# Kernel tuning notes

Measured on AMD Instinct MI355X. Metric: run time of the kernel, lower is better.

## Reference

```python
import jax, jax.numpy as jnp
import numpy as np

D_MODEL = 512
NHEAD = 8
HEAD_DIM = D_MODEL // NHEAD
D_FF = 2048
EPS = 1e-5


def _linear_params(key, d_in, d_out):
    kw, kb = jax.random.split(key)
    bound = 1.0 / np.sqrt(d_in)
    W = jax.random.uniform(kw, (d_out, d_in), jnp.float32, -bound, bound)
    b = jax.random.uniform(kb, (d_out,), jnp.float32, -bound, bound)
    return W, b


def setup_inputs() -> dict:
    key = jax.random.key(0)
    ks = jax.random.split(key, 8)
    src = jax.random.normal(ks[0], (4, 2048, D_MODEL), jnp.float32)
    Wq, bq = _linear_params(ks[1], D_MODEL, D_MODEL)
    Wk, bk = _linear_params(ks[2], D_MODEL, D_MODEL)
    Wv, bv = _linear_params(ks[3], D_MODEL, D_MODEL)
    Wo, bo = _linear_params(ks[4], D_MODEL, D_MODEL)
    W1, b1 = _linear_params(ks[5], D_MODEL, D_FF)
    W2, b2 = _linear_params(ks[6], D_FF, D_MODEL)
    g1 = jnp.ones((D_MODEL,), jnp.float32)
    be1 = jnp.zeros((D_MODEL,), jnp.float32)
    g2 = jnp.ones((D_MODEL,), jnp.float32)
    be2 = jnp.zeros((D_MODEL,), jnp.float32)
    return dict(src=src, Wq=Wq, bq=bq, Wk=Wk, bk=bk, Wv=Wv, bv=bv,
                Wo=Wo, bo=bo, W1=W1, b1=b1, W2=W2, b2=b2,
                g1=g1, be1=be1, g2=g2, be2=be2)


def _layer_norm(x, g, b):
    mu = jnp.mean(x, axis=-1, keepdims=True)
    var = jnp.mean(jnp.square(x - mu), axis=-1, keepdims=True)
    return (x - mu) / jnp.sqrt(var + EPS) * g + b


def reference(src, Wq, bq, Wk, bk, Wv, bv, Wo, bo, W1, b1, W2, b2, g1, be1, g2, be2):
    B, T, D = src.shape
    scale = np.sqrt(HEAD_DIM).astype(np.float32)
    # Projections (torch Linear: x @ W.T + b)
    Q = (src @ Wq.T + bq).reshape(B, T, NHEAD, HEAD_DIM).transpose(0, 2, 1, 3)
    K = (src @ Wk.T + bk).reshape(B, T, NHEAD, HEAD_DIM).transpose(0, 2, 1, 3)
    V = (src @ Wv.T + bv).reshape(B, T, NHEAD, HEAD_DIM).transpose(0, 2, 1, 3)
    # Explicit QK^T -> softmax -> V (no mask, dropout=0)
    scores = jnp.einsum('bhqd,bhkd->bhqk', Q, K) / scale  # (B,H,T,T)
    attn = jax.nn.softmax(scores, axis=-1)
    ctx = jnp.einsum('bhqk,bhkd->bhqd', attn, V)
    ctx = ctx.transpose(0, 2, 1, 3).reshape(B, T, D)
    attn_out = ctx @ Wo.T + bo
    # Add & Norm 1
    x = _layer_norm(src + attn_out, g1, be1)
    # FFN: Linear -> GELU -> Linear
    h = jax.nn.gelu(x @ W1.T + b1, approximate=False)
    ffn_out = h @ W2.T + b2
    # Add & Norm 2
    return _layer_norm(x + ffn_out, g2, be2)
```

## Files before the change

kernel.cpp:

```cpp
#include <hip/hip_runtime.h>
#include <hip/hip_bf16.h>
#include <math.h>

typedef __bf16 bf16_t;
typedef __bf16 bf16x8 __attribute__((ext_vector_type(8)));
typedef __bf16 bf16x2 __attribute__((ext_vector_type(2)));
typedef float  f32x4  __attribute__((ext_vector_type(4)));

#define D_MODEL 512
#define NHEAD   8
#define HD      64
#define D_FF    2048
#define TOKENS  8192
#define SEQ     2048
#define BATCH   4

__device__ __forceinline__ void gload16(const bf16_t* g, bf16_t* l)
{
    __builtin_amdgcn_global_load_lds(
        (const __attribute__((address_space(1))) void*)g,
        (__attribute__((address_space(3))) void*)l,
        16, 0, 0);
}

__device__ __forceinline__ void cvt4(const float* s, bf16_t* d)
{
    float4 v = *(const float4*)s;
    alignas(8) bf16_t t[4] = {(bf16_t)v.x, (bf16_t)v.y, (bf16_t)v.z, (bf16_t)v.w};
    *(uint2*)d = *(const uint2*)t;
}

__global__ void cvt_weights(const float* __restrict__ Wq, const float* __restrict__ Wk,
                            const float* __restrict__ Wv, const float* __restrict__ Wo,
                            const float* __restrict__ W1, const float* __restrict__ W2,
                            const float* __restrict__ bq, const float* __restrict__ bk,
                            const float* __restrict__ bv,
                            bf16_t* __restrict__ Wqkvb, bf16_t* __restrict__ Wob,
                            bf16_t* __restrict__ W1b, bf16_t* __restrict__ W2b,
                            float* __restrict__ bqkv, float* __restrict__ zbias)
{
    int i = blockIdx.x * 256 + threadIdx.x;
    if (i < 65536)        cvt4(Wq + (size_t)i * 4,            Wqkvb + (size_t)i * 4);
    else if (i < 131072)  cvt4(Wk + (size_t)(i - 65536) * 4,  Wqkvb + (size_t)i * 4);
    else if (i < 196608)  cvt4(Wv + (size_t)(i - 131072) * 4, Wqkvb + (size_t)i * 4);
    else if (i < 262144)  cvt4(Wo + (size_t)(i - 196608) * 4, Wob + (size_t)(i - 196608) * 4);
    else if (i < 524288)  cvt4(W1 + (size_t)(i - 262144) * 4, W1b + (size_t)(i - 262144) * 4);
    else if (i < 786432)  cvt4(W2 + (size_t)(i - 524288) * 4, W2b + (size_t)(i - 524288) * 4);
    else if (i < 786816) {
        int j = i - 786432;
        const float* s = (j < 128) ? bq + j * 4 : (j < 256) ? bk + (j - 128) * 4
                                                            : bv + (j - 256) * 4;
        *(float4*)(bqkv + (j & 127) * 4 + (j >> 7) * 512) = *(const float4*)s;
    } else if (i < 786944) {
        int j = i - 786816;
        *(float4*)(zbias + j * 4) = make_float4(0.f, 0.f, 0.f, 0.f);
    }
}

template <int BM, int EPI, bool AF32, bool SPLIT2>
__global__ __launch_bounds__(256)
void gemm_bt(const void* __restrict__ Ain, const bf16_t* __restrict__ B,
             const float* __restrict__ bias, const float* __restrict__ biasz,
             void* __restrict__ Cout, int M, int N, int K)
{
    constexpr int MI = BM / 32;
    __shared__ bf16_t sA[BM][32];
    __shared__ bf16_t sB[128][32];
    bf16_t* sAf = &sA[0][0];
    bf16_t* sBf = &sB[0][0];

    const int tid  = threadIdx.x;
    const int wave = tid >> 6;
    const int lane = tid & 63;
    const int g    = lane >> 4;
    const int c16  = lane & 15;
    const int wm   = (wave >> 1) * (BM / 2);
    const int wn   = (wave & 1) * 64;
    const int m0   = blockIdx.y * BM;
    const int n0   = blockIdx.x * 128;

    const int zz    = SPLIT2 ? blockIdx.z : 0;
    const int Keff  = SPLIT2 ? (K >> 1) : K;
    const int kbase = zz * Keff;
    const float* bptr = (SPLIT2 && zz) ? biasz : bias;

    const f32x4 fz = {0.f, 0.f, 0.f, 0.f};
    f32x4 acc[MI][4];
#pragma unroll
    for (int i = 0; i < MI; i++)
#pragma unroll
        for (int j = 0; j < 4; j++) acc[i][j] = fz;

    const int srow = tid >> 2;
    const int scol = (tid & 3) * 8;
    const bf16_t* pa  = AF32 ? nullptr : (const bf16_t*)Ain + (size_t)(m0 + srow) * K + kbase + scol;
    const float*  paf = AF32 ? (const float*)Ain + (size_t)(m0 + srow) * K + kbase + scol : nullptr;
    const bf16_t* pb  = B + (size_t)(n0 + srow) * K + kbase + scol;

    for (int k0 = 0; k0 < Keff; k0 += 32) {
        float4 ua[BM / 64][2];
        if (AF32) {
#pragma unroll
            for (int i = 0; i < BM / 64; i++) {
                ua[i][0] = *(const float4*)(paf + (size_t)i * 64 * K + k0);
                ua[i][1] = *(const float4*)(paf + (size_t)i * 64 * K + k0 + 4);
            }
        }
        __syncthreads();
        if (AF32) {
#pragma unroll
            for (int i = 0; i < BM / 64; i++) {
                alignas(16) bf16_t t[8];
#pragma unroll
                for (int j = 0; j < 4; j++) {
                    t[j]     = (bf16_t)((const float*)&ua[i][0])[j];
                    t[j + 4] = (bf16_t)((const float*)&ua[i][1])[j];
                }
                *(int4*)(sAf + i * 2048 + tid * 8) = *(const int4*)t;
            }
        } else {
#pragma unroll
            for (int i = 0; i < BM / 64; i++)
                gload16(pa + (size_t)i * 64 * K + k0, sAf + i * 2048 + tid * 8);
        }
#pragma unroll
        for (int i = 0; i < 2; i++)
            gload16(pb + (size_t)i * 64 * K + k0, sBf + i * 2048 + tid * 8);
        __syncthreads();

        bf16x8 af[MI], bfr[4];
#pragma unroll
        for (int i = 0; i < MI; i++)
            af[i] = *(const bf16x8*)&sA[wm + i * 16 + c16][g * 8];
#pragma unroll
        for (int j = 0; j < 4; j++)
            bfr[j] = *(const bf16x8*)&sB[wn + j * 16 + c16][g * 8];
#pragma unroll
        for (int mi = 0; mi < MI; mi++)
#pragma unroll
            for (int ni = 0; ni < 4; ni++)
                acc[mi][ni] = __builtin_amdgcn_mfma_f32_16x16x32_bf16(
                    af[mi], bfr[ni], acc[mi][ni], 0, 0, 0);
    }

    float* outf = (float*)Cout + (size_t)zz * M * N;
#pragma unroll
    for (int mi = 0; mi < MI; mi++) {
#pragma unroll
        for (int ni = 0; ni < 4; ni++) {
            const int col = n0 + wn + ni * 16 + c16;
            const float bv = bptr[col];
#pragma unroll
            for (int r = 0; r < 4; r++) {
                const int row = m0 + wm + mi * 16 + g * 4 + r;
                float v = acc[mi][ni][r] + bv;
                if (EPI == 1) v = 0.5f * v * (1.f + erff(v * 0.70710678118654752f));
                if (EPI == 2)
                    outf[(size_t)row * N + col] = v;
                else
                    ((bf16_t*)Cout)[(size_t)row * N + col] = (bf16_t)v;
            }
        }
    }
}

__global__ __launch_bounds__(256)
void transpose_v(const bf16_t* __restrict__ qkv, bf16_t* __restrict__ vt)
{
    __shared__ bf16_t st[64][72];
    const int t0 = blockIdx.x * 64;
    const int bh = blockIdx.y;
    const int b = bh >> 3, h = bh & 7;
    const int tid = threadIdx.x;

    for (int c = tid; c < 512; c += 256) {
        int r = c >> 3, cj = (c & 7) * 8;
        const bf16_t* src = qkv + ((size_t)(b * SEQ + t0 + r)) * 1536 + 1024 + h * 64 + cj;
        *(int4*)&st[r][cj] = *(const int4*)src;
    }
    __syncthreads();
    for (int c = tid; c < 512; c += 256) {
        int d = c >> 3, pj = (c & 7) * 8;
        alignas(16) bf16_t tmp[8];
#pragma unroll
        for (int j = 0; j < 8; j++) {
            int p = pj + j;
            int t = (p & 32) + ((p & 1) << 4) + ((p & 31) >> 1);
            tmp[j] = st[t][d];
        }
        *(int4*)(vt + ((size_t)(bh * 64 + d)) * SEQ + t0 + pj) = *(const int4*)tmp;
    }
}

__global__ __launch_bounds__(256)
void flash_attn(const bf16_t* __restrict__ qkv, const bf16_t* __restrict__ vt,
                bf16_t* __restrict__ ctx)
{
    __shared__ bf16_t sK[2][64][64];
    __shared__ bf16_t sVt[2][64][64];
    __shared__ bf16_t sOnes[16][72];
    __shared__ bf16_t sP[128][72];

    const int bh = blockIdx.y;
    const int b = bh >> 3, h = bh & 7;
    const int q0 = blockIdx.x * 128;
    const int tid = threadIdx.x;
    const int wave = tid >> 6, lane = tid & 63;
    const int g = lane >> 4, c16 = lane & 15;

    for (int c = tid; c < 16 * 72; c += 256)
        sOnes[c / 72][c % 72] = (c / 72 == 0) ? (bf16_t)1.0f : (bf16_t)0.0f;

    const float qscale = 0.125f * 1.4426950408889634f;
    bf16x8 aq[2][2];
#pragma unroll
    for (int mf = 0; mf < 2; mf++)
#pragma unroll
        for (int ks = 0; ks < 2; ks++) {
            bf16x8 v = *(const bf16x8*)(qkv +
                ((size_t)(b * SEQ + q0 + wave * 32 + mf * 16 + c16)) * 1536 +
                h * 64 + ks * 32 + g * 8);
#pragma unroll
            for (int j = 0; j < 8; j++) v[j] = (bf16_t)((float)v[j] * qscale);
            aq[mf][ks] = v;
        }

    const f32x4 fz = {0.f, 0.f, 0.f, 0.f};
    f32x4 acc_o[2][5];
#pragma unroll
    for (int mf = 0; mf < 2; mf++)
#pragma unroll
        for (int nd = 0; nd < 5; nd++) acc_o[mf][nd] = fz;

    const int f0 = tid,        r0 = f0 >> 3, l0 = (f0 & 7) ^ (r0 & 7);
    const int f1 = tid + 256,  r1 = f1 >> 3, l1 = (f1 & 7) ^ (r1 & 7);
    const bf16_t* gK0 = qkv + ((size_t)(b * SEQ + r0)) * 1536 + 512 + h * 64 + l0 * 8;
    const bf16_t* gK1 = qkv + ((size_t)(b * SEQ + r1)) * 1536 + 512 + h * 64 + l1 * 8;
    const bf16_t* gV0 = vt + ((size_t)(bh * 64 + r0)) * SEQ + l0 * 8;
    const bf16_t* gV1 = vt + ((size_t)(bh * 64 + r1)) * SEQ + l1 * 8;
    bf16_t* lK = &sK[0][0][0];
    bf16_t* lV = &sVt[0][0][0];

    gload16(gK0, lK + f0 * 8);
    gload16(gK1, lK + f1 * 8);
    gload16(gV0, lV + f0 * 8);
    gload16(gV1, lV + f1 * 8);

    for (int it = 0; it < 32; ++it) {
        const int cur = it & 1;
        __syncthreads();
        if (it < 31) {
            const size_t kv = (size_t)(it + 1) * 64;
            const int bo = (cur ^ 1) * 4096;
            gload16(gK0 + kv * 1536, lK + bo + f0 * 8);
            gload16(gK1 + kv * 1536, lK + bo + f1 * 8);
            gload16(gV0 + kv,        lV + bo + f0 * 8);
            gload16(gV1 + kv,        lV + bo + f1 * 8);
        }

        f32x4 accs[2][4];
#pragma unroll
        for (int mf = 0; mf < 2; mf++)
#pragma unroll
            for (int n = 0; n < 4; n++) accs[mf][n] = fz;
#pragma unroll
        for (int ks = 0; ks < 2; ks++)
#pragma unroll
            for (int n = 0; n < 4; n++) {
                const int pc = ((ks * 4 + g) ^ (c16 & 7)) * 8;
                bf16x8 bk = *(const bf16x8*)&sK[cur][n * 16 + c16][pc];
                accs[0][n] = __builtin_amdgcn_mfma_f32_16x16x32_bf16(aq[0][ks], bk, accs[0][n], 0, 0, 0);
                accs[1][n] = __builtin_amdgcn_mfma_f32_16x16x32_bf16(aq[1][ks], bk, accs[1][n], 0, 0, 0);
            }

#pragma unroll
        for (int mf = 0; mf < 2; mf++)
#pragma unroll
            for (int r = 0; r < 4; r++) {
                const int prow = wave * 32 + mf * 16 + g * 4 + r;
#pragma unroll
                for (int ks = 0; ks < 2; ks++) {
                    bf16x2 pp;
                    pp[0] = (bf16_t)__builtin_amdgcn_exp2f(accs[mf][2 * ks][r]);
                    pp[1] = (bf16_t)__builtin_amdgcn_exp2f(accs[mf][2 * ks + 1][r]);
                    *(bf16x2*)&sP[prow][ks * 32 + 2 * c16] = pp;
                }
            }

#pragma unroll
        for (int ks = 0; ks < 2; ks++) {
            bf16x8 ap0 = *(const bf16x8*)&sP[wave * 32 + c16][ks * 32 + g * 8];
            bf16x8 ap1 = *(const bf16x8*)&sP[wave * 32 + 16 + c16][ks * 32 + g * 8];
#pragma unroll
            for (int nd = 0; nd < 5; nd++) {
                bf16x8 vb;
                if (nd < 4) {
                    const int pc = ((ks * 4 + g) ^ (c16 & 7)) * 8;
                    vb = *(const bf16x8*)&sVt[cur][nd * 16 + c16][pc];
                } else {
                    vb = *(const bf16x8*)&sOnes[c16][ks * 32 + g * 8];
                }
                acc_o[0][nd] = __builtin_amdgcn_mfma_f32_16x16x32_bf16(ap0, vb, acc_o[0][nd], 0, 0, 0);
                acc_o[1][nd] = __builtin_amdgcn_mfma_f32_16x16x32_bf16(ap1, vb, acc_o[1][nd], 0, 0, 0);
            }
        }
    }

#pragma unroll
    for (int mf = 0; mf < 2; mf++)
#pragma unroll
        for (int r = 0; r < 4; r++) {
            float lv  = __shfl(acc_o[mf][4][r], lane & 48, 64);
            float inv = 1.0f / lv;
            const size_t base =
                ((size_t)(b * SEQ + q0 + wave * 32 + mf * 16 + g * 4 + r)) * 512 + h * 64;
#pragma unroll
            for (int nd = 0; nd < 4; nd++)
                ctx[base + nd * 16 + c16] = (bf16_t)(acc_o[mf][nd][r] * inv);
        }
}

__global__ __launch_bounds__(256)
void add_ln3(const float* __restrict__ a, const float* __restrict__ b,
             const float* __restrict__ c,
             const float* __restrict__ gamma, const float* __restrict__ beta,
             float* __restrict__ outf, bf16_t* __restrict__ outb)
{
    const int row  = blockIdx.x * 4 + (threadIdx.x >> 6);
    const int lane = threadIdx.x & 63;
    const size_t base = (size_t)row * 512 + lane * 8;

    float v[8];
#pragma unroll
    for (int h = 0; h < 2; h++) {
        float4 av = *(const float4*)(a + base + h * 4);
        float4 bv = *(const float4*)(b + base + h * 4);
        float4 cv = *(const float4*)(c + base + h * 4);
        v[h * 4 + 0] = av.x + bv.x + cv.x;
        v[h * 4 + 1] = av.y + bv.y + cv.y;
        v[h * 4 + 2] = av.z + bv.z + cv.z;
        v[h * 4 + 3] = av.w + bv.w + cv.w;
    }

    float s = 0.f;
#pragma unroll
    for (int i = 0; i < 8; i++) s += v[i];
#pragma unroll
    for (int off = 32; off > 0; off >>= 1) s += __shfl_xor(s, off);
    const float mu = s * (1.f / 512.f);

    float q = 0.f;
#pragma unroll
    for (int i = 0; i < 8; i++) { float d = v[i] - mu; q += d * d; }
#pragma unroll
    for (int off = 32; off > 0; off >>= 1) q += __shfl_xor(q, off);
    const float rstd = rsqrtf(q * (1.f / 512.f) + 1e-5f);

    float4 g0 = *(const float4*)(gamma + lane * 8);
    float4 g1 = *(const float4*)(gamma + lane * 8 + 4);
    float4 e0 = *(const float4*)(beta + lane * 8);
    float4 e1 = *(const float4*)(beta + lane * 8 + 4);
    const float gg[8] = {g0.x, g0.y, g0.z, g0.w, g1.x, g1.y, g1.z, g1.w};
    const float ee[8] = {e0.x, e0.y, e0.z, e0.w, e1.x, e1.y, e1.z, e1.w};

    float o[8];
#pragma unroll
    for (int i = 0; i < 8; i++) o[i] = (v[i] - mu) * rstd * gg[i] + ee[i];

    *(float4*)(outf + base)     = make_float4(o[0], o[1], o[2], o[3]);
    *(float4*)(outf + base + 4) = make_float4(o[4], o[5], o[6], o[7]);
    if (outb) {
        alignas(16) bf16_t ob[8];
#pragma unroll
        for (int i = 0; i < 8; i++) ob[i] = (bf16_t)o[i];
        *(int4*)(outb + base) = *(const int4*)ob;
    }
}

extern "C" void kernel_launch(void* const* d_in, const int* in_sizes, int n_in,
                              void* d_out, int out_size, void* d_ws, size_t ws_size,
                              hipStream_t stream)
{
    const float* src = (const float*)d_in[0];
    const float* Wq  = (const float*)d_in[1];  const float* bq  = (const float*)d_in[2];
    const float* Wk  = (const float*)d_in[3];  const float* bk  = (const float*)d_in[4];
    const float* Wv  = (const float*)d_in[5];  const float* bv  = (const float*)d_in[6];
    const float* Wo  = (const float*)d_in[7];  const float* bo  = (const float*)d_in[8];
    const float* W1  = (const float*)d_in[9];  const float* b1  = (const float*)d_in[10];
    const float* W2  = (const float*)d_in[11]; const float* b2  = (const float*)d_in[12];
    const float* g1  = (const float*)d_in[13]; const float* be1 = (const float*)d_in[14];
    const float* g2  = (const float*)d_in[15]; const float* be2 = (const float*)d_in[16];
    float* out = (float*)d_out;

    char* ws = (char*)d_ws;
    size_t off = 0;
    auto alloc = [&](size_t bytes) -> void* {
        void* p = ws + off;
        off = (off + bytes + 255) & ~(size_t)255;
        return p;
    };

    bf16_t* Wqkvb = (bf16_t*)alloc((size_t)1536 * 512 * 2);
    bf16_t* Wob   = (bf16_t*)alloc((size_t)512 * 512 * 2);
    bf16_t* W1b   = (bf16_t*)alloc((size_t)2048 * 512 * 2);
    bf16_t* W2b   = (bf16_t*)alloc((size_t)512 * 2048 * 2);
    float*  bqkv  = (float*)alloc(1536 * 4);
    float*  zbias = (float*)alloc(512 * 4);
    bf16_t* QKV   = (bf16_t*)alloc((size_t)TOKENS * 1536 * 2);
    bf16_t* Vt    = (bf16_t*)alloc((size_t)32 * 64 * SEQ * 2);
    bf16_t* CTX   = (bf16_t*)alloc((size_t)TOKENS * 512 * 2);
    float*  ATTa  = (float*)alloc((size_t)TOKENS * 512 * 4);
    float*  ATTb  = (float*)alloc((size_t)TOKENS * 512 * 4);
    float*  X1    = (float*)alloc((size_t)TOKENS * 512 * 4);
    bf16_t* X1b   = (bf16_t*)alloc((size_t)TOKENS * 512 * 2);

    bf16_t* H    = QKV;
    float*  FFNa = ATTa;
    float*  FFNb = ATTb;

    cvt_weights<<<3074, 256, 0, stream>>>(Wq, Wk, Wv, Wo, W1, W2, bq, bk, bv,
                                          Wqkvb, Wob, W1b, W2b, bqkv, zbias);

    gemm_bt<128, 0, true, false><<<dim3(12, 64), 256, 0, stream>>>(
        src, Wqkvb, bqkv, zbias, QKV, TOKENS, 1536, 512);

    transpose_v<<<dim3(32, 32), 256, 0, stream>>>(QKV, Vt);
    flash_attn<<<dim3(16, 32), 256, 0, stream>>>(QKV, Vt, CTX);

    gemm_bt<64, 2, false, true><<<dim3(4, 128, 2), 256, 0, stream>>>(
        CTX, Wob, bo, zbias, ATTa, TOKENS, 512, 512);

    add_ln3<<<2048, 256, 0, stream>>>(src, ATTa, ATTb, g1, be1, X1, X1b);

    gemm_bt<128, 1, false, false><<<dim3(16, 64), 256, 0, stream>>>(
        X1b, W1b, b1, zbias, H, TOKENS, 2048, 512);

    gemm_bt<64, 2, false, true><<<dim3(4, 128, 2), 256, 0, stream>>>(
        H, W2b, b2, zbias, FFNa, TOKENS, 512, 2048);

    add_ln3<<<2048, 256, 0, stream>>>(X1, FFNa, FFNb, g2, be2, out, nullptr);
}
```

Measured before the change: 309.2 us.

## Double-buffer GEMM LDS tiles and pre-convert src to bf16 in conversion kernel

The GEMM kernel gets a two-stage LDS ping-pong buffer. Async global-to-LDS loads for the next K tile are issued before the MFMA work on the current tile, and there is one barrier per iteration instead of two. To keep every GEMM on this path, src is now converted to bf16 inside the weight-conversion kernel, which removes the fp32 A-operand variant. This costs twice the LDS per block and an extra bf16 copy of src written and read through global memory. The code relies on the compiler inserting the needed vmcnt waits before the barrier for global_load_lds, which is a correctness risk.

Measured after the change: 296.5 us. -4.1%, faster.

```diff
diff --git a/kernel.cpp b/kernel.cpp
--- a/kernel.cpp
+++ b/kernel.cpp
@@ -30,16 +30,20 @@
     *(uint2*)d = *(const uint2*)t;
 }
 
-__global__ void cvt_weights(const float* __restrict__ Wq, const float* __restrict__ Wk,
+__global__ void cvt_weights(const float* __restrict__ src,
+                            const float* __restrict__ Wq, const float* __restrict__ Wk,
                             const float* __restrict__ Wv, const float* __restrict__ Wo,
                             const float* __restrict__ W1, const float* __restrict__ W2,
                             const float* __restrict__ bq, const float* __restrict__ bk,
                             const float* __restrict__ bv,
+                            bf16_t* __restrict__ Xb,
                             bf16_t* __restrict__ Wqkvb, bf16_t* __restrict__ Wob,
                             bf16_t* __restrict__ W1b, bf16_t* __restrict__ W2b,
                             float* __restrict__ bqkv, float* __restrict__ zbias)
 {
     int i = blockIdx.x * 256 + threadIdx.x;
+    if (i < 1048576) { cvt4(src + (size_t)i * 4, Xb + (size_t)i * 4); return; }
+    i -= 1048576;
     if (i < 65536)        cvt4(Wq + (size_t)i * 4,            Wqkvb + (size_t)i * 4);
     else if (i < 131072)  cvt4(Wk + (size_t)(i - 65536) * 4,  Wqkvb + (size_t)i * 4);
     else if (i < 196608)  cvt4(Wv + (size_t)(i - 131072) * 4, Wqkvb + (size_t)i * 4);
@@ -57,17 +61,17 @@
     }
 }
 
-template <int BM, int EPI, bool AF32, bool SPLIT2>
+template <int BM, int EPI, bool SPLIT2>
 __global__ __launch_bounds__(256)
-void gemm_bt(const void* __restrict__ Ain, const bf16_t* __restrict__ B,
+void gemm_bt(const bf16_t* __restrict__ A, const bf16_t* __restrict__ B,
              const float* __restrict__ bias, const float* __restrict__ biasz,
              void* __restrict__ Cout, int M, int N, int K)
 {
     constexpr int MI = BM / 32;
-    __shared__ bf16_t sA[BM][32];
-    __shared__ bf16_t sB[128][32];
-    bf16_t* sAf = &sA[0][0];
-    bf16_t* sBf = &sB[0][0];
+    __shared__ bf16_t sA[2][BM][32];
+    __shared__ bf16_t sB[2][128][32];
+    bf16_t* sAf = &sA[0][0][0];
+    bf16_t* sBf = &sB[0][0][0];
 
     const int tid  = threadIdx.x;
     const int wave = tid >> 6;
@@ -93,48 +97,39 @@
 
     const int srow = tid >> 2;
     const int scol = (tid & 3) * 8;
-    const bf16_t* pa  = AF32 ? nullptr : (const bf16_t*)Ain + (size_t)(m0 + srow) * K + kbase + scol;
-    const float*  paf = AF32 ? (const float*)Ain + (size_t)(m0 + srow) * K + kbase + scol : nullptr;
-    const bf16_t* pb  = B + (size_t)(n0 + srow) * K + kbase + scol;
-
-    for (int k0 = 0; k0 < Keff; k0 += 32) {
-        float4 ua[BM / 64][2];
-        if (AF32) {
-#pragma unroll
-            for (int i = 0; i < BM / 64; i++) {
-                ua[i][0] = *(const float4*)(paf + (size_t)i * 64 * K + k0);
-                ua[i][1] = *(const float4*)(paf + (size_t)i * 64 * K + k0 + 4);
-            }
-        }
+    const bf16_t* pa = A + (size_t)(m0 + srow) * K + kbase + scol;
+    const bf16_t* pb = B + (size_t)(n0 + srow) * K + kbase + scol;
+
+#pragma unroll
+    for (int i = 0; i < BM / 64; i++)
+        gload16(pa + (size_t)i * 64 * K, sAf + i * 2048 + tid * 8);
+#pragma unroll
+    for (int i = 0; i < 2; i++)
+        gload16(pb + (size_t)i * 64 * K, sBf + i * 2048 + tid * 8);
+
+    const int NK = Keff >> 5;
+    for (int kk = 0; kk < NK; ++kk) {
+        const int cur = kk & 1;
         __syncthreads();
-        if (AF32) {
-#pragma unroll
-            for (int i = 0; i < BM / 64; i++) {
-                alignas(16) bf16_t t[8];
-#pragma unroll
-                for (int j = 0; j < 4; j++) {
-                    t[j]     = (bf16_t)((const float*)&ua[i][0])[j];
-                    t[j + 4] = (bf16_t)((const float*)&ua[i][1])[j];
-                }
-                *(int4*)(sAf + i * 2048 + tid * 8) = *(const int4*)t;
-            }
-        } else {
+        if (kk + 1 < NK) {
+            const int k0 = (kk + 1) * 32;
+            bf16_t* dA = sAf + (cur ^ 1) * (BM * 32);
+            bf16_t* dB = sBf + (cur ^ 1) * 4096;
 #pragma unroll
             for (int i = 0; i < BM / 64; i++)
-                gload16(pa + (size_t)i * 64 * K + k0, sAf + i * 2048 + tid * 8);
-        }
-#pragma unroll
-        for (int i = 0; i < 2; i++)
-            gload16(pb + (size_t)i * 64 * K + k0, sBf + i * 2048 + tid * 8);
-        __syncthreads();
+                gload16(pa + (size_t)i * 64 * K + k0, dA + i * 2048 + tid * 8);
+#pragma unroll
+            for (int i = 0; i < 2; i++)
+                gload16(pb + (size_t)i * 64 * K + k0, dB + i * 2048 + tid * 8);
+        }
 
         bf16x8 af[MI], bfr[4];
 #pragma unroll
         for (int i = 0; i < MI; i++)
-            af[i] = *(const bf16x8*)&sA[wm + i * 16 + c16][g * 8];
+            af[i] = *(const bf16x8*)&sA[cur][wm + i * 16 + c16][g * 8];
 #pragma unroll
         for (int j = 0; j < 4; j++)
-            bfr[j] = *(const bf16x8*)&sB[wn + j * 16 + c16][g * 8];
+            bfr[j] = *(const bf16x8*)&sB[cur][wn + j * 16 + c16][g * 8];
 #pragma unroll
         for (int mi = 0; mi < MI; mi++)
 #pragma unroll
@@ -400,6 +395,7 @@
         return p;
     };
 
+    bf16_t* Xb    = (bf16_t*)alloc((size_t)TOKENS * 512 * 2);
     bf16_t* Wqkvb = (bf16_t*)alloc((size_t)1536 * 512 * 2);
     bf16_t* Wob   = (bf16_t*)alloc((size_t)512 * 512 * 2);
     bf16_t* W1b   = (bf16_t*)alloc((size_t)2048 * 512 * 2);
@@ -418,24 +414,24 @@
     float*  FFNa = ATTa;
     float*  FFNb = ATTb;
 
-    cvt_weights<<<3074, 256, 0, stream>>>(Wq, Wk, Wv, Wo, W1, W2, bq, bk, bv,
-                                          Wqkvb, Wob, W1b, W2b, bqkv, zbias);
-
-    gemm_bt<128, 0, true, false><<<dim3(12, 64), 256, 0, stream>>>(
-        src, Wqkvb, bqkv, zbias, QKV, TOKENS, 1536, 512);
+    cvt_weights<<<7170, 256, 0, stream>>>(src, Wq, Wk, Wv, Wo, W1, W2, bq, bk, bv,
+                                          Xb, Wqkvb, Wob, W1b, W2b, bqkv, zbias);
+
+    gemm_bt<128, 0, false><<<dim3(12, 64), 256, 0, stream>>>(
+        Xb, Wqkvb, bqkv, zbias, QKV, TOKENS, 1536, 512);
 
     transpose_v<<<dim3(32, 32), 256, 0, stream>>>(QKV, Vt);
     flash_attn<<<dim3(16, 32), 256, 0, stream>>>(QKV, Vt, CTX);
 
-    gemm_bt<64, 2, false, true><<<dim3(4, 128, 2), 256, 0, stream>>>(
+    gemm_bt<64, 2, true><<<dim3(4, 128, 2), 256, 0, stream>>>(
         CTX, Wob, bo, zbias, ATTa, TOKENS, 512, 512);
 
     add_ln3<<<2048, 256, 0, stream>>>(src, ATTa, ATTb, g1, be1, X1, X1b);
 
-    gemm_bt<128, 1, false, false><<<dim3(16, 64), 256, 0, stream>>>(
+    gemm_bt<128, 1, false><<<dim3(16, 64), 256, 0, stream>>>(
         X1b, W1b, b1, zbias, H, TOKENS, 2048, 512);
 
-    gemm_bt<64, 2, false, true><<<dim3(4, 128, 2), 256, 0, stream>>>(
+    gemm_bt<64, 2, true><<<dim3(4, 128, 2), 256, 0, stream>>>(
         H, W2b, b2, zbias, FFNa, TOKENS, 512, 2048);
 
     add_ln3<<<2048, 256, 0, stream>>>(X1, FFNa, FFNb, g2, be2, out, nullptr);
```
